# Kernel optimization log

Measured on AMD Instinct MI355X. Metric: run time of the kernel, lower is better.

Reference implementation:

```python
import jax, jax.numpy as jnp
import numpy as np

N_NODES = 100000
N_EDGES = 1600000
D_IN = 64
D_OUT = 64


def setup_inputs() -> dict:
    key = jax.random.key(0)
    k1, k2, k3, k4 = jax.random.split(key, 4)
    x = jax.random.normal(k1, (N_NODES, D_IN), dtype=jnp.float32)
    src = jax.random.randint(k2, (N_EDGES,), 0, N_NODES, dtype=jnp.int32)
    dst = jax.random.randint(k3, (N_EDGES,), 0, N_NODES, dtype=jnp.int32)
    W = jax.random.normal(k4, (D_OUT, D_IN), dtype=jnp.float32) / np.sqrt(D_IN)
    b = jnp.zeros((D_OUT,), dtype=jnp.float32)
    return {"x": x, "src": src, "dst": dst, "W": W, "b": b}


def reference(x, src, dst, W, b):
    # DGL SAGEConv with 'gcn' aggregator:
    #   h_neigh = (sum_{j in N_in(i)} x_j + x_i) / (in_degree(i) + 1)
    #   out     = h_neigh @ W^T + b
    N = x.shape[0]
    # gather source features and scatter-add into destination nodes  [N, D_IN]
    neigh_sum = jax.ops.segment_sum(x[src], dst, num_segments=N)
    deg = jax.ops.segment_sum(jnp.ones_like(dst, dtype=x.dtype), dst, num_segments=N)
    h_neigh = (neigh_sum + x) / (deg + 1.0)[:, None]
    return h_neigh @ W.T + b
```

## Files before the change

kernel.cpp:

```cpp
#include <hip/hip_runtime.h>

#define D 64
#define BSH 7
#define BSZ 128
#define NBMAX 1024
#define TILE 8192
#define CAP  3072

typedef unsigned int   uint;
typedef unsigned short ushort_t;
typedef __attribute__((ext_vector_type(8))) short bf16x8;
typedef __attribute__((ext_vector_type(4))) float f32x4;

__device__ __forceinline__ ushort_t f2bf(float f) {
    uint u = __float_as_uint(f);
    u += 0x7FFFu + ((u >> 16) & 1u);
    return (ushort_t)(u >> 16);
}

__global__ __launch_bounds__(256) void k_bhist(
    const int* __restrict__ dst, int* __restrict__ bucketCount,
    int* __restrict__ blockBase, const float4* __restrict__ x4,
    uint4* __restrict__ xb4, int n8, int nb, int n_edges)
{
    __shared__ int hist[NBMAX];
    const int tid = threadIdx.x;
    for (int i = tid; i < nb; i += 256) hist[i] = 0;
    __syncthreads();

    {
        const int chunk = (n8 + gridDim.x - 1) / gridDim.x;
        const int lo = blockIdx.x * chunk;
        const int hi = min(n8, lo + chunk);
        for (int t = lo + tid; t < hi; t += 256) {
            float4 a = x4[t * 2];
            float4 c = x4[t * 2 + 1];
            uint4 o;
            o.x = (uint)f2bf(a.x) | ((uint)f2bf(a.y) << 16);
            o.y = (uint)f2bf(a.z) | ((uint)f2bf(a.w) << 16);
            o.z = (uint)f2bf(c.x) | ((uint)f2bf(c.y) << 16);
            o.w = (uint)f2bf(c.z) | ((uint)f2bf(c.w) << 16);
            xb4[t] = o;
        }
    }

    const int e0 = blockIdx.x * TILE;
    const int n4 = n_edges >> 2;
    const int4* dst4 = (const int4*)dst;
#pragma unroll
    for (int k = 0; k < TILE / 1024; ++k) {
        int i4 = (e0 >> 2) + k * 256 + tid;
        if (i4 < n4) {
            int4 d = dst4[i4];
            atomicAdd(&hist[d.x >> BSH], 1);
            atomicAdd(&hist[d.y >> BSH], 1);
            atomicAdd(&hist[d.z >> BSH], 1);
            atomicAdd(&hist[d.w >> BSH], 1);
        }
    }
    if (blockIdx.x == gridDim.x - 1) {
        for (int e = (n4 << 2) + tid; e < n_edges; e += 256)
            atomicAdd(&hist[dst[e] >> BSH], 1);
    }
    __syncthreads();
    for (int i = tid; i < nb; i += 256)
        blockBase[(size_t)blockIdx.x * nb + i] = atomicAdd(&bucketCount[i], hist[i]);
}

__global__ __launch_bounds__(1024) void k_bscan(
    const int* __restrict__ bucketCount, int* __restrict__ bucketBase, int nb)
{
    __shared__ int s[1024];
    const int tid = threadIdx.x;
    int v = (tid < nb) ? bucketCount[tid] : 0;
    s[tid] = v;
    __syncthreads();
    for (int off = 1; off < 1024; off <<= 1) {
        int t = (tid >= off) ? s[tid - off] : 0;
        __syncthreads();
        s[tid] += t;
        __syncthreads();
    }
    if (tid <= nb) bucketBase[tid] = s[tid] - v;
}

__global__ __launch_bounds__(256) void k_bscatter(
    const int* __restrict__ src, const int* __restrict__ dst,
    const int* __restrict__ bucketBase, const int* __restrict__ blockBase,
    int* __restrict__ packed, int nb, int n_edges)
{
    __shared__ int cur[NBMAX];
    const int tid = threadIdx.x;
    const int blk = blockIdx.x;
    for (int i = tid; i < nb; i += 256)
        cur[i] = bucketBase[i] + blockBase[(size_t)blk * nb + i];
    __syncthreads();

    const int e0 = blk * TILE;
    const int n4 = n_edges >> 2;
    const int4* src4 = (const int4*)src;
    const int4* dst4 = (const int4*)dst;
#pragma unroll
    for (int k = 0; k < TILE / 1024; ++k) {
        int i4 = (e0 >> 2) + k * 256 + tid;
        if (i4 < n4) {
            int4 sv = src4[i4];
            int4 dv = dst4[i4];
            int p;
            p = atomicAdd(&cur[dv.x >> BSH], 1); packed[p] = sv.x | ((dv.x & (BSZ-1)) << 24);
            p = atomicAdd(&cur[dv.y >> BSH], 1); packed[p] = sv.y | ((dv.y & (BSZ-1)) << 24);
            p = atomicAdd(&cur[dv.z >> BSH], 1); packed[p] = sv.z | ((dv.z & (BSZ-1)) << 24);
            p = atomicAdd(&cur[dv.w >> BSH], 1); packed[p] = sv.w | ((dv.w & (BSZ-1)) << 24);
        }
    }
    if (blk == gridDim.x - 1) {
        for (int e = (n4 << 2) + tid; e < n_edges; e += 256) {
            int p = atomicAdd(&cur[dst[e] >> BSH], 1);
            packed[p] = src[e] | ((dst[e] & (BSZ-1)) << 24);
        }
    }
}

__global__ __launch_bounds__(512, 8) void k_aggcsr(
    const int* __restrict__ packed, const int* __restrict__ bucketBase,
    const uint2* __restrict__ xb2, const float* __restrict__ W,
    const float* __restrict__ bvec, float* __restrict__ out, int n_nodes)
{
    __shared__ int pool[2 * CAP + 128];
    __shared__ ushort_t Wl[64 * 64];
    __shared__ int ldeg[BSZ];
    __shared__ int lofs[BSZ];
    __shared__ int cur[BSZ];

    int* raw = pool;
    int* srt = pool + CAP;

    const int tid = threadIdx.x;
    const int bucket = blockIdx.x;
    const int ebase = bucketBase[bucket];
    const int ecnt  = bucketBase[bucket + 1] - ebase;
    const bool fits = (ecnt <= CAP);
    const uint nmax = (uint)(n_nodes - 1);

    {
        const int o = tid >> 3;
        const int j = (tid & 7) * 8;
        const float* wp = W + o * 64 + j;
        float4 wa = *(const float4*)wp;
        float4 wb = *(const float4*)(wp + 4);
        uint4 w4;
        w4.x = (uint)f2bf(wa.x) | ((uint)f2bf(wa.y) << 16);
        w4.y = (uint)f2bf(wa.z) | ((uint)f2bf(wa.w) << 16);
        w4.z = (uint)f2bf(wb.x) | ((uint)f2bf(wb.y) << 16);
        w4.w = (uint)f2bf(wb.z) | ((uint)f2bf(wb.w) << 16);
        *(uint4*)((char*)Wl + o * 128 + ((j * 2) ^ ((o & 7) << 4))) = w4;
    }
    if (tid < BSZ) ldeg[tid] = 0;
    __syncthreads();

    if (fits) {
        for (int i = tid; i < ecnt; i += 512) {
            int pk = packed[ebase + i];
            raw[i] = pk;
            atomicAdd(&ldeg[((uint)pk) >> 24], 1);
        }
    } else {
        for (int i = tid; i < ecnt; i += 512)
            atomicAdd(&ldeg[((uint)packed[ebase + i]) >> 24], 1);
    }
    __syncthreads();

    {
        int v = 0;
        if (tid < BSZ) { v = ldeg[tid]; lofs[tid] = v; }
        __syncthreads();
        for (int off = 1; off < BSZ; off <<= 1) {
            int t = (tid < BSZ && tid >= off) ? lofs[tid - off] : 0;
            __syncthreads();
            if (tid < BSZ) lofs[tid] += t;
            __syncthreads();
        }
        if (tid < BSZ) { int e = lofs[tid] - v; lofs[tid] = e; cur[tid] = e; }
    }
    __syncthreads();

    if (fits) {
        for (int i = tid; i < ecnt; i += 512) {
            int pk = raw[i];
            int pos = atomicAdd(&cur[((uint)pk) >> 24], 1);
            srt[pos] = pk & 0x00FFFFFF;
        }
    }
    __syncthreads();

    const int wave = tid >> 6;
    const int lane = tid & 63;
    const int g    = lane >> 4;
    const int fq   = lane & 15;

#define CVLO(u) __uint_as_float((u) << 16)
#define CVHI(u) __uint_as_float((u) & 0xFFFF0000u)

    uint2 hreg[4];
#pragma unroll
    for (int p = 0; p < 4; ++p) { hreg[p].x = 0u; hreg[p].y = 0u; }

#pragma unroll
    for (int p = 0; p < 4; ++p) {
        const int nl = wave * 16 + p * 4 + g;
        const int node = (bucket << BSH) + nl;
        const bool valid = (node < n_nodes);
        const int cnt = valid ? ldeg[nl] : 0;
        const int eb  = valid ? lofs[nl] : 0;

        int cm = max(cnt, __shfl_xor(cnt, 16, 64));
        cm = max(cm, __shfl_xor(cm, 32, 64));

        float s0 = 0.f, s1 = 0.f, s2 = 0.f, s3 = 0.f;

        if (fits) {
            for (int i = 0; i < cm; i += 4) {
                int v0 = srt[eb + i];
                int v1 = srt[eb + i + 1];
                int v2 = srt[eb + i + 2];
                int v3 = srt[eb + i + 3];
                float m0 = (i     < cnt) ? 1.0f : 0.0f;
                float m1 = (i + 1 < cnt) ? 1.0f : 0.0f;
                float m2 = (i + 2 < cnt) ? 1.0f : 0.0f;
                float m3 = (i + 3 < cnt) ? 1.0f : 0.0f;
                uint2 A0 = xb2[(size_t)min((uint)v0, nmax) * 16 + fq];
                uint2 A1 = xb2[(size_t)min((uint)v1, nmax) * 16 + fq];
                uint2 A2 = xb2[(size_t)min((uint)v2, nmax) * 16 + fq];
                uint2 A3 = xb2[(size_t)min((uint)v3, nmax) * 16 + fq];
                s0 = fmaf(m0, CVLO(A0.x), s0);
                s1 = fmaf(m0, CVHI(A0.x), s1);
                s2 = fmaf(m0, CVLO(A0.y), s2);
                s3 = fmaf(m0, CVHI(A0.y), s3);
                s0 = fmaf(m1, CVLO(A1.x), s0);
                s1 = fmaf(m1, CVHI(A1.x), s1);
                s2 = fmaf(m1, CVLO(A1.y), s2);
                s3 = fmaf(m1, CVHI(A1.y), s3);
                s0 = fmaf(m2, CVLO(A2.x), s0);
                s1 = fmaf(m2, CVHI(A2.x), s1);
                s2 = fmaf(m2, CVLO(A2.y), s2);
                s3 = fmaf(m2, CVHI(A2.y), s3);
                s0 = fmaf(m3, CVLO(A3.x), s0);
                s1 = fmaf(m3, CVHI(A3.x), s1);
                s2 = fmaf(m3, CVLO(A3.y), s2);
                s3 = fmaf(m3, CVHI(A3.y), s3);
            }
        } else {
            const int nlm = valid ? nl : -1;
            for (int i = 0; i < ecnt; ++i) {
                int pk = packed[ebase + i];
                float m0 = ((int)(((uint)pk) >> 24) == nlm) ? 1.0f : 0.0f;
                uint2 A0 = xb2[(size_t)min((uint)(pk & 0x00FFFFFF), nmax) * 16 + fq];
                s0 = fmaf(m0, CVLO(A0.x), s0);
                s1 = fmaf(m0, CVHI(A0.x), s1);
                s2 = fmaf(m0, CVLO(A0.y), s2);
                s3 = fmaf(m0, CVHI(A0.y), s3);
            }
        }

        if (valid) {
            uint2 xv = xb2[(size_t)node * 16 + fq];
            float rinv = 1.0f / (float)(cnt + 1);
            float h0 = (s0 + CVLO(xv.x)) * rinv;
            float h1 = (s1 + CVHI(xv.x)) * rinv;
            float h2 = (s2 + CVLO(xv.y)) * rinv;
            float h3 = (s3 + CVHI(xv.y)) * rinv;
            hreg[p].x = (uint)f2bf(h0) | ((uint)f2bf(h1) << 16);
            hreg[p].y = (uint)f2bf(h2) | ((uint)f2bf(h3) << 16);
        }
    }
#undef CVLO
#undef CVHI

    __syncthreads();

    char* hwb = (char*)pool + wave * 2048;
#pragma unroll
    for (int p = 0; p < 4; ++p) {
        int nl = p * 4 + g;
        *(uint2*)(hwb + nl * 128 + ((fq * 8) ^ ((nl & 7) << 4))) = hreg[p];
    }

    const int m  = lane & 15;
    const int kg = lane >> 4;
    bf16x8 a0 = *(const bf16x8*)(hwb + m * 128 + (((kg * 16)     ) ^ ((m & 7) << 4)));
    bf16x8 a1 = *(const bf16x8*)(hwb + m * 128 + (((64 + kg * 16)) ^ ((m & 7) << 4)));

    const int node0 = (bucket << BSH) + wave * 16;
#pragma unroll
    for (int c = 0; c < 4; ++c) {
        const int o = c * 16 + m;
        bf16x8 b0 = *(const bf16x8*)((char*)Wl + o * 128 + (((kg * 16)     ) ^ ((o & 7) << 4)));
        bf16x8 b1 = *(const bf16x8*)((char*)Wl + o * 128 + (((64 + kg * 16)) ^ ((o & 7) << 4)));
        f32x4 acc = {0.f, 0.f, 0.f, 0.f};
        acc = __builtin_amdgcn_mfma_f32_16x16x32_bf16(a0, b0, acc, 0, 0, 0);
        acc = __builtin_amdgcn_mfma_f32_16x16x32_bf16(a1, b1, acc, 0, 0, 0);
        const float bias = bvec[o];
#pragma unroll
        for (int r = 0; r < 4; ++r) {
            int row = node0 + kg * 4 + r;
            if (row < n_nodes)
                out[(size_t)row * 64 + o] = acc[r] + bias;
        }
    }
}

extern "C" void kernel_launch(void* const* d_in, const int* in_sizes, int n_in,
                              void* d_out, int out_size, void* d_ws, size_t ws_size,
                              hipStream_t stream)
{
    const float* x   = (const float*)d_in[0];
    const int*   src = (const int*)d_in[1];
    const int*   dst = (const int*)d_in[2];
    const float* W   = (const float*)d_in[3];
    const float* b   = (const float*)d_in[4];
    float* out = (float*)d_out;

    const int n_nodes = in_sizes[0] / D;
    const int n_edges = in_sizes[1];
    const int nb  = (n_nodes + BSZ - 1) >> BSH;
    const int nbA = (n_edges + TILE - 1) / TILE;

    ushort_t* xb = (ushort_t*)d_ws;
    int* bucketCount = (int*)(xb + (size_t)n_nodes * D);
    int* bucketBase  = bucketCount + NBMAX;
    int* blockBase   = bucketBase + NBMAX + 1;
    int* packed      = blockBase + (size_t)nbA * nb;

    hipMemsetAsync(bucketCount, 0, NBMAX * sizeof(int), stream);

    const int n8 = n_nodes * D / 8;
    k_bhist   <<<nbA, 256, 0, stream>>>(dst, bucketCount, blockBase,
                                        (const float4*)x, (uint4*)xb, n8, nb, n_edges);
    k_bscan   <<<1,  1024, 0, stream>>>(bucketCount, bucketBase, nb);
    k_bscatter<<<nbA, 256, 0, stream>>>(src, dst, bucketBase, blockBase, packed, nb, n_edges);
    k_aggcsr  <<<nb,  512, 0, stream>>>(packed, bucketBase, (const uint2*)xb,
                                        W, b, out, n_nodes);
}
```

Measured before the change: 81.66 us.

## Fuse bucket scan into scatter kernel, shrink edge tile, unroll gather by eight

Removes the separate single-block scan kernel. Every scatter block now recomputes the bucket prefix sum in shared memory, and block zero writes bucketBase for the aggregation kernel. The edge tile shrinks from 8192 to 2048, which gives more histogram and scatter blocks but a larger blockBase array. The gather loop in the aggregation kernel loads eight neighbours per iteration instead of four, putting more loads in flight. The pool is padded because the eight-wide loop reads past each node's edge range.

```diff
diff --git a/kernel.cpp b/kernel.cpp
--- a/kernel.cpp
+++ b/kernel.cpp
@@ -4,7 +4,7 @@
 #define BSH 7
 #define BSZ 128
 #define NBMAX 1024
-#define TILE 8192
+#define TILE 2048
 #define CAP  3072
 
 typedef unsigned int   uint;
@@ -67,33 +67,49 @@
         blockBase[(size_t)blockIdx.x * nb + i] = atomicAdd(&bucketCount[i], hist[i]);
 }
 
-__global__ __launch_bounds__(1024) void k_bscan(
-    const int* __restrict__ bucketCount, int* __restrict__ bucketBase, int nb)
-{
-    __shared__ int s[1024];
-    const int tid = threadIdx.x;
-    int v = (tid < nb) ? bucketCount[tid] : 0;
-    s[tid] = v;
-    __syncthreads();
-    for (int off = 1; off < 1024; off <<= 1) {
-        int t = (tid >= off) ? s[tid - off] : 0;
-        __syncthreads();
-        s[tid] += t;
-        __syncthreads();
-    }
-    if (tid <= nb) bucketBase[tid] = s[tid] - v;
-}
-
 __global__ __launch_bounds__(256) void k_bscatter(
     const int* __restrict__ src, const int* __restrict__ dst,
-    const int* __restrict__ bucketBase, const int* __restrict__ blockBase,
-    int* __restrict__ packed, int nb, int n_edges)
+    const int* __restrict__ bucketCount, const int* __restrict__ blockBase,
+    int* __restrict__ bucketBase, int* __restrict__ packed,
+    int nb, int n_edges)
 {
+    __shared__ int sc[NBMAX];
     __shared__ int cur[NBMAX];
+    __shared__ int ts[256];
     const int tid = threadIdx.x;
     const int blk = blockIdx.x;
+
+    {
+        const int base = tid * 4;
+        int v[4];
+#pragma unroll
+        for (int k = 0; k < 4; ++k)
+            v[k] = (base + k < nb) ? bucketCount[base + k] : 0;
+        int tsum = v[0] + v[1] + v[2] + v[3];
+        ts[tid] = tsum;
+        __syncthreads();
+        for (int off = 1; off < 256; off <<= 1) {
+            int t = (tid >= off) ? ts[tid - off] : 0;
+            __syncthreads();
+            ts[tid] += t;
+            __syncthreads();
+        }
+        int run = ts[tid] - tsum;
+#pragma unroll
+        for (int k = 0; k < 4; ++k) {
+            if (base + k < nb) sc[base + k] = run;
+            run += v[k];
+        }
+    }
+    __syncthreads();
+
+    if (blk == 0) {
+        for (int i = tid; i <= nb; i += 256)
+            bucketBase[i] = (i < nb) ? sc[i] : n_edges;
+    }
+
     for (int i = tid; i < nb; i += 256)
-        cur[i] = bucketBase[i] + blockBase[(size_t)blk * nb + i];
+        cur[i] = sc[i] + blockBase[(size_t)blk * nb + i];
     __syncthreads();
 
     const int e0 = blk * TILE;
@@ -126,7 +142,7 @@
     const uint2* __restrict__ xb2, const float* __restrict__ W,
     const float* __restrict__ bvec, float* __restrict__ out, int n_nodes)
 {
-    __shared__ int pool[2 * CAP + 128];
+    __shared__ int pool[2 * CAP + 136];
     __shared__ ushort_t Wl[64 * 64];
     __shared__ int ldeg[BSZ];
     __shared__ int lofs[BSZ];
@@ -201,6 +217,8 @@
 #define CVLO(u) __uint_as_float((u) << 16)
 #define CVHI(u) __uint_as_float((u) & 0xFFFF0000u)
 
+    const uint2* __restrict__ xbf = xb2 + fq;
+
     uint2 hreg[4];
 #pragma unroll
     for (int p = 0; p < 4; ++p) { hreg[p].x = 0u; hreg[p].y = 0u; }
@@ -219,42 +237,29 @@
         float s0 = 0.f, s1 = 0.f, s2 = 0.f, s3 = 0.f;
 
         if (fits) {
-            for (int i = 0; i < cm; i += 4) {
-                int v0 = srt[eb + i];
-                int v1 = srt[eb + i + 1];
-                int v2 = srt[eb + i + 2];
-                int v3 = srt[eb + i + 3];
-                float m0 = (i     < cnt) ? 1.0f : 0.0f;
-                float m1 = (i + 1 < cnt) ? 1.0f : 0.0f;
-                float m2 = (i + 2 < cnt) ? 1.0f : 0.0f;
-                float m3 = (i + 3 < cnt) ? 1.0f : 0.0f;
-                uint2 A0 = xb2[(size_t)min((uint)v0, nmax) * 16 + fq];
-                uint2 A1 = xb2[(size_t)min((uint)v1, nmax) * 16 + fq];
-                uint2 A2 = xb2[(size_t)min((uint)v2, nmax) * 16 + fq];
-                uint2 A3 = xb2[(size_t)min((uint)v3, nmax) * 16 + fq];
-                s0 = fmaf(m0, CVLO(A0.x), s0);
-                s1 = fmaf(m0, CVHI(A0.x), s1);
-                s2 = fmaf(m0, CVLO(A0.y), s2);
-                s3 = fmaf(m0, CVHI(A0.y), s3);
-                s0 = fmaf(m1, CVLO(A1.x), s0);
-                s1 = fmaf(m1, CVHI(A1.x), s1);
-                s2 = fmaf(m1, CVLO(A1.y), s2);
-                s3 = fmaf(m1, CVHI(A1.y), s3);
-                s0 = fmaf(m2, CVLO(A2.x), s0);
-                s1 = fmaf(m2, CVHI(A2.x), s1);
-                s2 = fmaf(m2, CVLO(A2.y), s2);
-                s3 = fmaf(m2, CVHI(A2.y), s3);
-                s0 = fmaf(m3, CVLO(A3.x), s0);
-                s1 = fmaf(m3, CVHI(A3.x), s1);
-                s2 = fmaf(m3, CVLO(A3.y), s2);
-                s3 = fmaf(m3, CVHI(A3.y), s3);
+            for (int i = 0; i < cm; i += 8) {
+                int vv[8];
+#pragma unroll
+                for (int k = 0; k < 8; ++k) vv[k] = srt[eb + i + k];
+                uint2 A[8];
+#pragma unroll
+                for (int k = 0; k < 8; ++k)
+                    A[k] = xbf[(size_t)min((uint)vv[k], nmax) * 16];
+#pragma unroll
+                for (int k = 0; k < 8; ++k) {
+                    float m = (i + k < cnt) ? 1.0f : 0.0f;
+                    s0 = fmaf(m, CVLO(A[k].x), s0);
+                    s1 = fmaf(m, CVHI(A[k].x), s1);
+                    s2 = fmaf(m, CVLO(A[k].y), s2);
+                    s3 = fmaf(m, CVHI(A[k].y), s3);
+                }
             }
         } else {
             const int nlm = valid ? nl : -1;
             for (int i = 0; i < ecnt; ++i) {
                 int pk = packed[ebase + i];
                 float m0 = ((int)(((uint)pk) >> 24) == nlm) ? 1.0f : 0.0f;
-                uint2 A0 = xb2[(size_t)min((uint)(pk & 0x00FFFFFF), nmax) * 16 + fq];
+                uint2 A0 = xbf[(size_t)min((uint)(pk & 0x00FFFFFF), nmax) * 16];
                 s0 = fmaf(m0, CVLO(A0.x), s0);
                 s1 = fmaf(m0, CVHI(A0.x), s1);
                 s2 = fmaf(m0, CVLO(A0.y), s2);
@@ -263,7 +268,7 @@
         }
 
         if (valid) {
-            uint2 xv = xb2[(size_t)node * 16 + fq];
+            uint2 xv = xbf[(size_t)node * 16];
             float rinv = 1.0f / (float)(cnt + 1);
             float h0 = (s0 + CVLO(xv.x)) * rinv;
             float h1 = (s1 + CVHI(xv.x)) * rinv;
@@ -336,8 +341,8 @@
     const int n8 = n_nodes * D / 8;
     k_bhist   <<<nbA, 256, 0, stream>>>(dst, bucketCount, blockBase,
                                         (const float4*)x, (uint4*)xb, n8, nb, n_edges);
-    k_bscan   <<<1,  1024, 0, stream>>>(bucketCount, bucketBase, nb);
-    k_bscatter<<<nbA, 256, 0, stream>>>(src, dst, bucketBase, blockBase, packed, nb, n_edges);
+    k_bscatter<<<nbA, 256, 0, stream>>>(src, dst, bucketCount, blockBase,
+                                        bucketBase, packed, nb, n_edges);
     k_aggcsr  <<<nb,  512, 0, stream>>>(packed, bucketBase, (const uint2*)xb,
                                         W, b, out, n_nodes);
 }
```

After: 96.06 us. 1.18x slower.
